# Kernel optimization log

Measured on AMD Instinct MI355X. Metric: run time of the kernel, lower is better.

The kernel has to match this reference:

```python
import jax, jax.numpy as jnp
import numpy as np

B, T, DIM, H = 2048, 16, 512, 8
INNER = 4 * DIM  # GEGLU inner dim
NUM_REL = 2 * T - 1


def _ln(x, g, b, eps=1e-5):
    m = jnp.mean(x, -1, keepdims=True)
    v = jnp.var(x, -1, keepdims=True)
    return (x - m) * jax.lax.rsqrt(v + eps) * g + b


def _temporal_attn(x, mask, g, b, wq, wk, wv, wo, bo, pe):
    # x: (B, T, C); mask: (1, T, T) bool; pe: (2T-1, C)
    Bn, Tn, C = x.shape
    d = C // H
    scale = d ** -0.5
    res = x
    xn = _ln(x, g, b)
    q = (xn @ wq).reshape(Bn, Tn, H, d).transpose(0, 2, 1, 3)  # (B,H,T,d)
    k = (xn @ wk).reshape(Bn, Tn, H, d).transpose(0, 2, 1, 3)
    v = (xn @ wv).reshape(Bn, Tn, H, d).transpose(0, 2, 1, 3)
    sim = jnp.einsum('bhmd,bhnd->bhmn', q, k)
    # contextual(2) relative position bias: project rel-pos embeddings through to_q/to_k
    rel = jnp.arange(Tn)[None, :] - jnp.arange(Tn)[:, None] + (Tn - 1)  # (T,T) in [0, 2T-2]
    P = pe[rel]                              # (T, T, C)
    Kr = (P @ wk).reshape(Tn, Tn, H, d)      # (T, T, H, d)
    Qr = (P @ wq).reshape(Tn, Tn, H, d)
    bias = jnp.einsum('bhmd,mnhd->bhmn', q, Kr) + jnp.einsum('bhnd,mnhd->bhmn', k, Qr)
    sim = (sim + bias) * scale
    sim = jnp.where(mask[:, None], sim, -jnp.finfo(sim.dtype).max)
    attn = jax.nn.softmax(sim, axis=-1)
    out = jnp.einsum('bhmn,bhnd->bhmd', attn, v)
    out = out.transpose(0, 2, 1, 3).reshape(Bn, Tn, C)
    return out @ wo + bo + res


def _geglu_ff(x, g, b, w1, b1, w2, b2):
    xn = _ln(x, g, b)
    h = xn @ w1 + b1                         # (B, T, 2*INNER)
    a, gate = jnp.split(h, 2, axis=-1)
    y = a * jax.nn.gelu(gate, approximate=False)
    return y @ w2 + b2 + x


def setup_inputs() -> dict:
    key = jax.random.key(0)
    ks = jax.random.split(key, 24)
    s = 0.02
    d = {
        'x': jax.random.normal(ks[0], (B, T, DIM), jnp.float32),
        'femb': jax.random.normal(ks[1], (T, DIM), jnp.float32),
        'attn_mask': jnp.ones((1, T, T), dtype=bool),
    }
    for i, base in [(2, '1'), (10, '2')]:
        d['n%s_g' % base] = jnp.ones((DIM,), jnp.float32)
        d['n%s_b' % base] = jnp.zeros((DIM,), jnp.float32)
        d['wq%s' % base] = jax.random.normal(ks[i], (DIM, DIM), jnp.float32) * s
        d['wk%s' % base] = jax.random.normal(ks[i + 1], (DIM, DIM), jnp.float32) * s
        d['wv%s' % base] = jax.random.normal(ks[i + 2], (DIM, DIM), jnp.float32) * s
        d['wo%s' % base] = jax.random.normal(ks[i + 3], (DIM, DIM), jnp.float32) * s
        d['bo%s' % base] = jnp.zeros((DIM,), jnp.float32)
        d['pe%s' % base] = jax.random.normal(ks[i + 4], (NUM_REL, DIM), jnp.float32) * s
    d['n3_g'] = jnp.ones((DIM,), jnp.float32)
    d['n3_b'] = jnp.zeros((DIM,), jnp.float32)
    d['ffw1'] = jax.random.normal(ks[20], (DIM, 2 * INNER), jnp.float32) * s
    d['ffb1'] = jnp.zeros((2 * INNER,), jnp.float32)
    d['ffw2'] = jax.random.normal(ks[21], (INNER, DIM), jnp.float32) * s
    d['ffb2'] = jnp.zeros((DIM,), jnp.float32)
    return d


def reference(x, femb,
              n1_g, n1_b, wq1, wk1, wv1, wo1, bo1, pe1,
              n2_g, n2_b, wq2, wk2, wv2, wo2, bo2, pe2,
              n3_g, n3_b, ffw1, ffb1, ffw2, ffb2,
              attn_mask):
    # femb is accepted but unused, matching TemporalTransformerBlock._forward
    x = _temporal_attn(x, attn_mask, n1_g, n1_b, wq1, wk1, wv1, wo1, bo1, pe1)
    x = _temporal_attn(x, attn_mask, n2_g, n2_b, wq2, wk2, wv2, wo2, bo2, pe2)
    x = _geglu_ff(x, n3_g, n3_b, ffw1, ffb1, ffw2, ffb2)
    return x
```

## Files before the change

### kernel.cpp

```cpp
#include <hip/hip_runtime.h>

typedef unsigned int uint;
typedef unsigned short ushort;

typedef float f32x4 __attribute__((ext_vector_type(4)));
typedef short bf16x8 __attribute__((ext_vector_type(8)));

using gas1 = const uint __attribute__((address_space(1)))*;
using las3 = uint __attribute__((address_space(3)))*;

static constexpr int TB    = 2048;
static constexpr int TT    = 16;
static constexpr int TD    = 512;
static constexpr int TH    = 8;
static constexpr int HD    = 64;
static constexpr int NROWS = TB * TT;
static constexpr int NREL  = 2 * TT - 1;
static constexpr int INNER = 2048;

__device__ __forceinline__ float bf2f(uint h) {
    union { uint u; float f; } x; x.u = h << 16; return x.f;
}
__device__ __forceinline__ ushort f2bf(float f) {
    union { float f; uint u; } x; x.f = f;
    uint r = x.u + 0x7fffu + ((x.u >> 16) & 1u);
    return (ushort)(r >> 16);
}
__device__ __forceinline__ void unpack8(uint4 v, float* f) {
    f[0] = bf2f(v.x & 0xffffu); f[1] = bf2f(v.x >> 16);
    f[2] = bf2f(v.y & 0xffffu); f[3] = bf2f(v.y >> 16);
    f[4] = bf2f(v.z & 0xffffu); f[5] = bf2f(v.z >> 16);
    f[6] = bf2f(v.w & 0xffffu); f[7] = bf2f(v.w >> 16);
}
__device__ __forceinline__ uint pck(float a, float b) {
    return (uint)f2bf(a) | ((uint)f2bf(b) << 16);
}
__device__ __forceinline__ uint4 pack8(const float* f) {
    return make_uint4(pck(f[0], f[1]), pck(f[2], f[3]), pck(f[4], f[5]), pck(f[6], f[7]));
}
__device__ __forceinline__ bool is_f32(const uint* probe) { return probe[0] == 0x3F800000u; }
__device__ __forceinline__ float ldraw(const void* p, size_t i, bool f32) {
    return f32 ? ((const float*)p)[i] : bf2f(((const ushort*)p)[i]);
}

struct TrP { const void* in[8]; ushort* out[8]; };
__global__ __launch_bounds__(256)
void tr8_k(TrP p, const uint* __restrict__ probe) {
    const bool f32 = is_f32(probe);
    const void* in  = p.in[blockIdx.z];
    ushort*     out = p.out[blockIdx.z];
    __shared__ ushort t[32][33];
    const int bx = blockIdx.x, by = blockIdx.y;
    const int x = threadIdx.x, y = threadIdx.y;
    #pragma unroll
    for (int i = 0; i < 4; ++i) {
        const size_t src = (size_t)(by * 32 + y + i * 8) * TD + bx * 32 + x;
        t[y + i * 8][x] = f32 ? f2bf(((const float*)in)[src]) : ((const ushort*)in)[src];
    }
    __syncthreads();
    #pragma unroll
    for (int i = 0; i < 4; ++i)
        out[(size_t)(bx * 32 + y + i * 8) * TD + by * 32 + x] = t[x][y + i * 8];
}

__global__ __launch_bounds__(256)
void transpose_k(const void* __restrict__ in, ushort* __restrict__ out, int R, int C,
                 const uint* __restrict__ probe) {
    const bool f32 = is_f32(probe);
    __shared__ ushort t[32][33];
    const int bx = blockIdx.x, by = blockIdx.y;
    const int x = threadIdx.x, y = threadIdx.y;
    #pragma unroll
    for (int i = 0; i < 4; ++i) {
        const size_t src = (size_t)(by * 32 + y + i * 8) * C + bx * 32 + x;
        t[y + i * 8][x] = f32 ? f2bf(((const float*)in)[src]) : ((const ushort*)in)[src];
    }
    __syncthreads();
    #pragma unroll
    for (int i = 0; i < 4; ++i)
        out[(size_t)(bx * 32 + y + i * 8) * R + by * 32 + x] = t[x][y + i * 8];
}

struct PewP { const void* pe[4]; const void* w[4]; ushort* out[4]; };
__global__ __launch_bounds__(256)
void pew4_k(PewP p, const uint* __restrict__ probe) {
    const bool f32 = is_f32(probe);
    const int z = blockIdx.z;
    const void* pe = p.pe[z];
    const void* w  = p.w[z];
    ushort*    out = p.out[z];
    const int c = blockIdx.x * 256 + threadIdx.x;
    const int r = blockIdx.y;
    float acc = 0.f;
    for (int k = 0; k < TD; ++k)
        acc += ldraw(pe, (size_t)r * TD + k, f32) * ldraw(w, (size_t)k * TD + c, f32);
    out[r * TD + c] = f2bf(acc);
}

template<bool RAW>
__global__ __launch_bounds__(256)
void ln_k(const void* __restrict__ xin, const void* __restrict__ gw,
          const void* __restrict__ bw, ushort* __restrict__ out,
          const uint* __restrict__ probe) {
    const bool f32 = is_f32(probe);
    const int row = blockIdx.x * 4 + (threadIdx.x >> 6);
    const int l = threadIdx.x & 63;
    const int c0 = l * 8;
    float v[8];
    if (RAW && f32) {
        const float* x = (const float*)xin + (size_t)row * TD + c0;
        const float4 a = *(const float4*)x;
        const float4 b = *(const float4*)(x + 4);
        v[0] = a.x; v[1] = a.y; v[2] = a.z; v[3] = a.w;
        v[4] = b.x; v[5] = b.y; v[6] = b.z; v[7] = b.w;
    } else {
        unpack8(*(const uint4*)((const ushort*)xin + (size_t)row * TD + c0), v);
    }
    float s = 0.f, s2 = 0.f;
    #pragma unroll
    for (int j = 0; j < 8; ++j) { s += v[j]; s2 += v[j] * v[j]; }
    #pragma unroll
    for (int off = 32; off; off >>= 1) {
        s  += __shfl_xor(s, off);
        s2 += __shfl_xor(s2, off);
    }
    const float mean = s * (1.f / TD);
    const float var  = s2 * (1.f / TD) - mean * mean;
    const float rstd = rsqrtf(var + 1e-5f);
    float gf[8], bf[8], r[8];
    if (f32) {
        const float* g = (const float*)gw + c0;
        const float* b = (const float*)bw + c0;
        #pragma unroll
        for (int j = 0; j < 8; ++j) { gf[j] = g[j]; bf[j] = b[j]; }
    } else {
        unpack8(*(const uint4*)((const ushort*)gw + c0), gf);
        unpack8(*(const uint4*)((const ushort*)bw + c0), bf);
    }
    #pragma unroll
    for (int j = 0; j < 8; ++j) r[j] = (v[j] - mean) * rstd * gf[j] + bf[j];
    *(uint4*)(out + (size_t)row * TD + c0) = pack8(r);
}

template<bool GEGLU>
__global__ __launch_bounds__(256)
void gemm_bt(const ushort* __restrict__ A, const ushort* __restrict__ Bt,
             const void* __restrict__ bias, const void* Res, void* C,
             int M, int N, int K, int resraw, int outraw, int outrow0,
             const uint* __restrict__ probe) {
    const bool f32 = is_f32(probe);
    constexpr int BN = GEGLU ? 64 : 128;
    constexpr int NI = GEGLU ? 2 : 4;
    __shared__ ushort sA[3][128 * 32];
    __shared__ ushort sB[3][BN * 32];
    __shared__ ushort sB2[GEGLU ? 3 : 1][GEGLU ? BN * 32 : 16];

    const int tid = threadIdx.x;

    const int lin = blockIdx.y * gridDim.x + blockIdx.x;
    const int cgx = gridDim.x >> 3;
    const int xcd = lin & 7;
    const int idx = lin >> 3;
    const int bx  = xcd * cgx + (idx % cgx);
    const int by  = idx / cgx;

    const int m0 = bx * 128;
    const int n0 = by * BN;
    const int w  = tid >> 6;
    const int l  = tid & 63;
    const int wm = (w >> 1) * 64;
    const int wn = (w & 1) * (BN / 2);
    const int fr = l & 15;
    const int fg = l >> 4;

    const int srow = tid >> 2;
    const int gsp  = (((tid & 3) ^ ((srow >> 1) & 3))) * 8;
    const ushort* gA0 = A  + (size_t)(m0 + srow) * K + gsp;
    const ushort* gA1 = gA0 + (size_t)64 * K;
    const ushort* gB0 = Bt + (size_t)(n0 + srow) * K + gsp;
    const ushort* gB1 = gB0 + (size_t)64 * K;
    const ushort* gG0 = Bt + (size_t)(N + n0 + srow) * K + gsp;

    f32x4 acc[4][NI]  = {};
    f32x4 acc2[4][NI] = {};

    const int NT = K >> 5;

    auto stage = [&](int t, int buf) {
        const int kt = t * 32;
        __builtin_amdgcn_global_load_lds((gas1)(const void*)(gA0 + kt),
            (las3)(void*)(&sA[buf][tid * 8]), 16, 0, 0);
        __builtin_amdgcn_global_load_lds((gas1)(const void*)(gA1 + kt),
            (las3)(void*)(&sA[buf][(tid + 256) * 8]), 16, 0, 0);
        __builtin_amdgcn_global_load_lds((gas1)(const void*)(gB0 + kt),
            (las3)(void*)(&sB[buf][tid * 8]), 16, 0, 0);
        if constexpr (!GEGLU)
            __builtin_amdgcn_global_load_lds((gas1)(const void*)(gB1 + kt),
                (las3)(void*)(&sB[buf][(tid + 256) * 8]), 16, 0, 0);
        if constexpr (GEGLU)
            __builtin_amdgcn_global_load_lds((gas1)(const void*)(gG0 + kt),
                (las3)(void*)(&sB2[buf][tid * 8]), 16, 0, 0);
    };
    auto lofs = [](int r, int g) { return (r * 4 + (g ^ ((r >> 1) & 3))) * 8; };

    stage(0, 0);
    stage(1, 1);
    asm volatile("s_waitcnt vmcnt(4)" ::: "memory");
    __builtin_amdgcn_s_barrier();

    for (int t = 0; t < NT; ++t) {
        const int cur = t % 3;
        if (t + 2 < NT) stage(t + 2, (t + 2) % 3);
        __builtin_amdgcn_sched_barrier(0);

        bf16x8 af[4], bn[NI], bg[NI];
        #pragma unroll
        for (int i = 0; i < 4; ++i)
            af[i] = *(const bf16x8*)&sA[cur][lofs(wm + i * 16 + fr, fg)];
        #pragma unroll
        for (int i = 0; i < NI; ++i) {
            bn[i] = *(const bf16x8*)&sB[cur][lofs(wn + i * 16 + fr, fg)];
            if constexpr (GEGLU)
                bg[i] = *(const bf16x8*)&sB2[cur][lofs(wn + i * 16 + fr, fg)];
        }
        #pragma unroll
        for (int mi = 0; mi < 4; ++mi)
            #pragma unroll
            for (int ni = 0; ni < NI; ++ni) {
                acc[mi][ni] = __builtin_amdgcn_mfma_f32_16x16x32_bf16(af[mi], bn[ni], acc[mi][ni], 0, 0, 0);
                if constexpr (GEGLU)
                    acc2[mi][ni] = __builtin_amdgcn_mfma_f32_16x16x32_bf16(af[mi], bg[ni], acc2[mi][ni], 0, 0, 0);
            }
        __builtin_amdgcn_sched_barrier(0);
        if (t + 2 < NT) {
            asm volatile("s_waitcnt vmcnt(4)" ::: "memory");
        } else {
            asm volatile("s_waitcnt vmcnt(0)" ::: "memory");
        }
        __builtin_amdgcn_s_barrier();
    }

    #pragma unroll
    for (int mi = 0; mi < 4; ++mi)
        #pragma unroll
        for (int ni = 0; ni < NI; ++ni) {
            const int col = n0 + wn + ni * 16 + fr;
            const float bv = bias ? ldraw(bias, col, f32) : 0.f;
            float bgv = 0.f;
            if constexpr (GEGLU) bgv = bias ? ldraw(bias, (size_t)N + col, f32) : 0.f;
            #pragma unroll
            for (int j = 0; j < 4; ++j) {
                const int row = m0 + wm + mi * 16 + fg * 4 + j;
                const size_t idx2 = (size_t)(outrow0 + row) * N + col;
                float v = acc[mi][ni][j] + bv;
                if constexpr (GEGLU) {
                    const float gt = acc2[mi][ni][j] + bgv;
                    v = v * (0.5f * gt * (1.f + erff(gt * 0.70710678118654752f)));
                }
                if (Res) v += resraw ? ldraw(Res, idx2, f32) : bf2f(((const ushort*)Res)[idx2]);
                if (outraw && f32) ((float*)C)[idx2] = v;
                else               ((ushort*)C)[idx2] = f2bf(v);
            }
        }
}

__global__ __launch_bounds__(64)
void attn_k(const ushort* __restrict__ qkv, const ushort* __restrict__ peWk,
            const ushort* __restrict__ peWq, ushort* __restrict__ out) {
    __shared__ ushort sQ[16][72], sK[16][72], sV[16][72];
    __shared__ ushort sPk[31][72], sPq[31][72];
    __shared__ float sP[16][20];

    const int tid = threadIdx.x;
    const int b = blockIdx.x >> 3;
    const int h = blockIdx.x & 7;
    const size_t rowbase = (size_t)b * 16 * (3 * TD) + h * HD;

    #pragma unroll
    for (int it = 0; it < 2; ++it) {
        const int c = tid + it * 64;
        const int m = c >> 3, part = c & 7;
        const ushort* src = qkv + rowbase + (size_t)m * (3 * TD) + part * 8;
        *(uint4*)&sQ[m][part * 8] = *(const uint4*)(src);
        *(uint4*)&sK[m][part * 8] = *(const uint4*)(src + TD);
        *(uint4*)&sV[m][part * 8] = *(const uint4*)(src + 2 * TD);
    }
    #pragma unroll
    for (int it = 0; it < 4; ++it) {
        const int c = tid + it * 64;
        if (c < NREL * 8) {
            const int r = c >> 3, part = c & 7;
            *(uint4*)&sPk[r][part * 8] = *(const uint4*)&peWk[(size_t)r * TD + h * HD + part * 8];
            *(uint4*)&sPq[r][part * 8] = *(const uint4*)&peWq[(size_t)r * TD + h * HD + part * 8];
        }
    }
    __syncthreads();

    const int m = tid & 15;
    const int g = tid >> 4;

    float aqk[4] = {0, 0, 0, 0}, ab1[4] = {0, 0, 0, 0}, ab2[4] = {0, 0, 0, 0};
    for (int dc = 0; dc < 8; ++dc) {
        float qf[8];
        unpack8(*(const uint4*)&sQ[m][dc * 8], qf);
        #pragma unroll
        for (int t = 0; t < 4; ++t) {
            const int n = g * 4 + t;
            const int rel = n - m + (TT - 1);
            float kf[8], pk[8], pq[8];
            unpack8(*(const uint4*)&sK[n][dc * 8], kf);
            unpack8(*(const uint4*)&sPk[rel][dc * 8], pk);
            unpack8(*(const uint4*)&sPq[rel][dc * 8], pq);
            #pragma unroll
            for (int j = 0; j < 8; ++j) {
                aqk[t] += qf[j] * kf[j];
                ab1[t] += qf[j] * pk[j];
                ab2[t] += kf[j] * pq[j];
            }
        }
    }
    float sim[4];
    #pragma unroll
    for (int t = 0; t < 4; ++t) sim[t] = (aqk[t] + ab1[t] + ab2[t]) * 0.125f;

    float mx = fmaxf(fmaxf(sim[0], sim[1]), fmaxf(sim[2], sim[3]));
    mx = fmaxf(mx, __shfl_xor(mx, 16));
    mx = fmaxf(mx, __shfl_xor(mx, 32));
    float e[4], ssum = 0.f;
    #pragma unroll
    for (int t = 0; t < 4; ++t) { e[t] = __expf(sim[t] - mx); ssum += e[t]; }
    ssum += __shfl_xor(ssum, 16);
    ssum += __shfl_xor(ssum, 32);
    const float inv = 1.f / ssum;
    #pragma unroll
    for (int t = 0; t < 4; ++t) sP[m][g * 4 + t] = e[t] * inv;
    __syncthreads();

    float o[16] = {};
    for (int n = 0; n < 16; ++n) {
        const float pv = sP[m][n];
        float vf[16];
        unpack8(*(const uint4*)&sV[n][g * 16], vf);
        unpack8(*(const uint4*)&sV[n][g * 16 + 8], vf + 8);
        #pragma unroll
        for (int i = 0; i < 16; ++i) o[i] += pv * vf[i];
    }
    ushort* dst = out + (size_t)(b * 16 + m) * TD + h * HD + g * 16;
    *(uint4*)dst = pack8(o);
    *(uint4*)(dst + 8) = pack8(o + 8);
}

extern "C" void kernel_launch(void* const* d_in, const int* in_sizes, int n_in,
                              void* d_out, int out_size, void* d_ws, size_t ws_size,
                              hipStream_t stream) {
    (void)in_sizes; (void)n_in; (void)out_size;

    const void* X   = d_in[0];
    const void* n1g = d_in[3];
    const void* n1b = d_in[4];
    const void* wq1 = d_in[5];
    const void* wk1 = d_in[6];
    const void* wv1 = d_in[7];
    const void* wo1 = d_in[8];
    const void* bo1 = d_in[9];
    const void* pe1 = d_in[10];
    const void* n2g = d_in[11];
    const void* n2b = d_in[12];
    const void* wq2 = d_in[13];
    const void* wk2 = d_in[14];
    const void* wv2 = d_in[15];
    const void* wo2 = d_in[16];
    const void* bo2 = d_in[17];
    const void* pe2 = d_in[18];
    const void* n3g = d_in[19];
    const void* n3b = d_in[20];
    const void* fw1 = d_in[21];
    const void* fb1 = d_in[22];
    const void* fw2 = d_in[23];
    const void* fb2 = d_in[24];
    const uint* probe = (const uint*)n1g;

    ushort* ws    = (ushort*)d_ws;
    ushort* xn    = ws;
    ushort* qkv   = xn + (size_t)NROWS * TD;
    ushort* x12   = qkv + (size_t)NROWS * (3 * TD);
    ushort* p     = x12 + (size_t)NROWS * TD;
    ushort* qkvT1 = p; p += (size_t)3 * TD * TD;
    ushort* woT1  = p; p += (size_t)TD * TD;
    ushort* qkvT2 = p; p += (size_t)3 * TD * TD;
    ushort* woT2  = p; p += (size_t)TD * TD;
    ushort* w1T   = p; p += (size_t)2 * INNER * TD;
    ushort* w2T   = p; p += (size_t)TD * INNER;
    ushort* peWk1 = p; p += NREL * TD;
    ushort* peWq1 = p; p += NREL * TD;
    ushort* peWk2 = p; p += NREL * TD;
    ushort* peWq2 = p; p += NREL * TD;
    const size_t need_bytes = (size_t)(p - ws) * sizeof(ushort);
    if (ws_size < need_bytes) return;

    ushort* aout = xn;
    ushort* ybuf = qkv;

    const dim3 tpb(32, 8);
    TrP trp;
    trp.in[0] = wq1; trp.out[0] = qkvT1;
    trp.in[1] = wk1; trp.out[1] = qkvT1 + TD * TD;
    trp.in[2] = wv1; trp.out[2] = qkvT1 + 2 * TD * TD;
    trp.in[3] = wo1; trp.out[3] = woT1;
    trp.in[4] = wq2; trp.out[4] = qkvT2;
    trp.in[5] = wk2; trp.out[5] = qkvT2 + TD * TD;
    trp.in[6] = wv2; trp.out[6] = qkvT2 + 2 * TD * TD;
    trp.in[7] = wo2; trp.out[7] = woT2;
    tr8_k<<<dim3(TD / 32, TD / 32, 8), tpb, 0, stream>>>(trp, probe);
    transpose_k<<<dim3(2 * INNER / 32, TD / 32), tpb, 0, stream>>>(fw1, w1T, TD, 2 * INNER, probe);
    transpose_k<<<dim3(TD / 32, INNER / 32), tpb, 0, stream>>>(fw2, w2T, INNER, TD, probe);
    PewP pwp;
    pwp.pe[0] = pe1; pwp.w[0] = wk1; pwp.out[0] = peWk1;
    pwp.pe[1] = pe1; pwp.w[1] = wq1; pwp.out[1] = peWq1;
    pwp.pe[2] = pe2; pwp.w[2] = wk2; pwp.out[2] = peWk2;
    pwp.pe[3] = pe2; pwp.w[3] = wq2; pwp.out[3] = peWq2;
    pew4_k<<<dim3(2, NREL, 4), 256, 0, stream>>>(pwp, probe);

    const int gm = NROWS / 128;

    ln_k<true><<<NROWS / 4, 256, 0, stream>>>(X, n1g, n1b, xn, probe);
    gemm_bt<false><<<dim3(gm, 12), 256, 0, stream>>>(
        xn, qkvT1, nullptr, nullptr, qkv, NROWS, 3 * TD, TD, 0, 0, 0, probe);
    attn_k<<<TB * TH, 64, 0, stream>>>(qkv, peWk1, peWq1, aout);
    gemm_bt<false><<<dim3(gm, 4), 256, 0, stream>>>(
        aout, woT1, bo1, X, x12, NROWS, TD, TD, 1, 0, 0, probe);

    ln_k<false><<<NROWS / 4, 256, 0, stream>>>(x12, n2g, n2b, xn, probe);
    gemm_bt<false><<<dim3(gm, 12), 256, 0, stream>>>(
        xn, qkvT2, nullptr, nullptr, qkv, NROWS, 3 * TD, TD, 0, 0, 0, probe);
    attn_k<<<TB * TH, 64, 0, stream>>>(qkv, peWk2, peWq2, aout);
    gemm_bt<false><<<dim3(gm, 4), 256, 0, stream>>>(
        aout, woT2, bo2, x12, x12, NROWS, TD, TD, 0, 0, 0, probe);

    ln_k<false><<<NROWS / 4, 256, 0, stream>>>(x12, n3g, n3b, xn, probe);
    const int chunk = NROWS / 2;
    for (int hh = 0; hh < 2; ++hh) {
        gemm_bt<true><<<dim3(chunk / 128, INNER / 64), 256, 0, stream>>>(
            xn + (size_t)hh * chunk * TD, w1T, fb1, nullptr, ybuf,
            chunk, INNER, TD, 0, 0, 0, probe);
        gemm_bt<false><<<dim3(chunk / 128, TD / 128), 256, 0, stream>>>(
            ybuf, w2T, fb2, (const void*)x12, d_out,
            chunk, TD, INNER, 0, 1, hh * chunk, probe);
    }
}
```

Before: 959.8 us.

## Add 256x256-tile 8-wave GEMM kernel for QKV, output and FF2 projections

```diff
diff --git a/kernel.cpp b/kernel.cpp
--- a/kernel.cpp
+++ b/kernel.cpp
@@ -140,6 +140,103 @@
     #pragma unroll
     for (int j = 0; j < 8; ++j) r[j] = (v[j] - mean) * rstd * gf[j] + bf[j];
     *(uint4*)(out + (size_t)row * TD + c0) = pack8(r);
+}
+
+__global__ __launch_bounds__(512)
+void gemm8_k(const ushort* __restrict__ A, const ushort* __restrict__ Bt,
+             const void* __restrict__ bias, const void* Res, void* C,
+             int M, int N, int K, int resraw, int outraw, int outrow0,
+             const uint* __restrict__ probe) {
+    const bool f32 = is_f32(probe);
+    __shared__ ushort sA[2][256 * 32];
+    __shared__ ushort sB[2][256 * 32];
+
+    const int tid = threadIdx.x;
+
+    const int lin = blockIdx.y * gridDim.x + blockIdx.x;
+    const int cgx = gridDim.x >> 3;
+    const int xcd = lin & 7;
+    const int idx = lin >> 3;
+    const int bx  = xcd * cgx + (idx % cgx);
+    const int by  = idx / cgx;
+    const int m0 = bx * 256, n0 = by * 256;
+
+    const int wv = tid >> 6, l = tid & 63;
+    const int wm = (wv >> 2) * 128;
+    const int wn = (wv & 3) * 64;
+    const int fr = l & 15, fg = l >> 4;
+
+    const int rl = tid >> 2;
+    const int sw = (tid & 3) ^ ((rl >> 1) & 3);
+    const ushort* gA = A  + (size_t)(m0 + rl) * K + sw * 8;
+    const ushort* gB = Bt + (size_t)(n0 + rl) * K + sw * 8;
+
+    f32x4 acc[8][4] = {};
+    const int NT = K >> 5;
+
+    auto stage_q = [&](int q, int t, int buf) {
+        const int g = q & 1;
+        if (q < 2)
+            __builtin_amdgcn_global_load_lds(
+                (gas1)(const void*)(gA + ((size_t)(g * 128) * K + t * 32)),
+                (las3)(void*)(&sA[buf][(g * 512 + tid) * 8]), 16, 0, 0);
+        else
+            __builtin_amdgcn_global_load_lds(
+                (gas1)(const void*)(gB + ((size_t)(g * 128) * K + t * 32)),
+                (las3)(void*)(&sB[buf][(g * 512 + tid) * 8]), 16, 0, 0);
+    };
+    auto lofs = [](int r, int s) { return (r * 4 + (s ^ ((r >> 1) & 3))) * 8; };
+
+    #pragma unroll
+    for (int q = 0; q < 4; ++q) stage_q(q, 0, 0);
+
+    for (int t = 0; t < NT; ++t) {
+        const int buf = t & 1;
+        bf16x8 bn[4];
+        #pragma unroll
+        for (int q = 0; q < 4; ++q) {
+            if (t + 1 < NT) stage_q(q, t + 1, buf ^ 1);
+            if (q == 0) {
+                if (t + 1 < NT) asm volatile("s_waitcnt vmcnt(1)" ::: "memory");
+                else            asm volatile("s_waitcnt vmcnt(0)" ::: "memory");
+                __builtin_amdgcn_s_barrier();
+                asm volatile("" ::: "memory");
+                #pragma unroll
+                for (int ni = 0; ni < 4; ++ni)
+                    bn[ni] = *(const bf16x8*)&sB[buf][lofs(wn + ni * 16 + fr, fg)];
+            }
+            bf16x8 af[2];
+            #pragma unroll
+            for (int mi2 = 0; mi2 < 2; ++mi2)
+                af[mi2] = *(const bf16x8*)&sA[buf][lofs(wm + (q * 2 + mi2) * 16 + fr, fg)];
+            __builtin_amdgcn_s_setprio(1);
+            #pragma unroll
+            for (int mi2 = 0; mi2 < 2; ++mi2)
+                #pragma unroll
+                for (int ni = 0; ni < 4; ++ni)
+                    acc[q * 2 + mi2][ni] = __builtin_amdgcn_mfma_f32_16x16x32_bf16(
+                        af[mi2], bn[ni], acc[q * 2 + mi2][ni], 0, 0, 0);
+            __builtin_amdgcn_s_setprio(0);
+            if (q == 3) { __builtin_amdgcn_s_barrier(); asm volatile("" ::: "memory"); }
+        }
+    }
+
+    #pragma unroll
+    for (int mi = 0; mi < 8; ++mi)
+        #pragma unroll
+        for (int ni = 0; ni < 4; ++ni) {
+            const int col = n0 + wn + ni * 16 + fr;
+            const float bv = bias ? ldraw(bias, col, f32) : 0.f;
+            #pragma unroll
+            for (int j = 0; j < 4; ++j) {
+                const int row = m0 + wm + mi * 16 + fg * 4 + j;
+                const size_t idx2 = (size_t)(outrow0 + row) * N + col;
+                float v = acc[mi][ni][j] + bv;
+                if (Res) v += resraw ? ldraw(Res, idx2, f32) : bf2f(((const ushort*)Res)[idx2]);
+                if (outraw && f32) ((float*)C)[idx2] = v;
+                else               ((ushort*)C)[idx2] = f2bf(v);
+            }
+        }
 }
 
 template<bool GEGLU>
@@ -421,20 +518,18 @@
     pwp.pe[3] = pe2; pwp.w[3] = wq2; pwp.out[3] = peWq2;
     pew4_k<<<dim3(2, NREL, 4), 256, 0, stream>>>(pwp, probe);
 
-    const int gm = NROWS / 128;
-
     ln_k<true><<<NROWS / 4, 256, 0, stream>>>(X, n1g, n1b, xn, probe);
-    gemm_bt<false><<<dim3(gm, 12), 256, 0, stream>>>(
+    gemm8_k<<<dim3(NROWS / 256, 6), 512, 0, stream>>>(
         xn, qkvT1, nullptr, nullptr, qkv, NROWS, 3 * TD, TD, 0, 0, 0, probe);
     attn_k<<<TB * TH, 64, 0, stream>>>(qkv, peWk1, peWq1, aout);
-    gemm_bt<false><<<dim3(gm, 4), 256, 0, stream>>>(
+    gemm8_k<<<dim3(NROWS / 256, 2), 512, 0, stream>>>(
         aout, woT1, bo1, X, x12, NROWS, TD, TD, 1, 0, 0, probe);
 
     ln_k<false><<<NROWS / 4, 256, 0, stream>>>(x12, n2g, n2b, xn, probe);
-    gemm_bt<false><<<dim3(gm, 12), 256, 0, stream>>>(
+    gemm8_k<<<dim3(NROWS / 256, 6), 512, 0, stream>>>(
         xn, qkvT2, nullptr, nullptr, qkv, NROWS, 3 * TD, TD, 0, 0, 0, probe);
     attn_k<<<TB * TH, 64, 0, stream>>>(qkv, peWk2, peWq2, aout);
-    gemm_bt<false><<<dim3(gm, 4), 256, 0, stream>>>(
+    gemm8_k<<<dim3(NROWS / 256, 2), 512, 0, stream>>>(
         aout, woT2, bo2, x12, x12, NROWS, TD, TD, 0, 0, 0, probe);
 
     ln_k<false><<<NROWS / 4, 256, 0, stream>>>(x12, n3g, n3b, xn, probe);
@@ -443,7 +538,7 @@
         gemm_bt<true><<<dim3(chunk / 128, INNER / 64), 256, 0, stream>>>(
             xn + (size_t)hh * chunk * TD, w1T, fb1, nullptr, ybuf,
             chunk, INNER, TD, 0, 0, 0, probe);
-        gemm_bt<false><<<dim3(chunk / 128, TD / 128), 256, 0, stream>>>(
+        gemm8_k<<<dim3(chunk / 256, 2), 512, 0, stream>>>(
             ybuf, w2T, fb2, (const void*)x12, d_out,
             chunk, TD, INNER, 0, 1, hh * chunk, probe);
     }
```

Result: slower. 1.010 ms (+5.3%).
